# Kernel tuning notes

Measured on AMD Instinct MI355X. Metric: run time of the kernel, lower is better.

## Reference

```python
import jax, jax.numpy as jnp
import numpy as np

HEAD_DIM = 4  # hard-coded by rosa_4bit_layer's reshape(B, T, -1, 4)


def setup_inputs() -> dict:
    key = jax.random.key(0)
    B, T, C = 4, 4096, 512
    kq, kk, kv = jax.random.split(key, 3)
    xq = jax.random.normal(kq, (B, T, C), dtype=jnp.float32)
    xk = jax.random.normal(kk, (B, T, C), dtype=jnp.float32)
    xv = jax.random.normal(kv, (B, T, C), dtype=jnp.float32)
    emb = jnp.ones((1, 1, C), dtype=jnp.float32)  # nn.Parameter(torch.ones((1,1,C)))
    return {"xq": xq, "xk": xk, "xv": xv, "emb": emb}


def _rosa_sufa(q, k, v):
    # q,k,v: (B, H, T, d) with d = 4.
    # Causal linear-attention recurrence with per-head d x d state:
    #   S_t = S_{t-1} + k_t v_t^T ;  o_t = q_t^T S_t
    # expressed as a cumulative sum over outer products (vectorized over T).
    kv = jnp.cumsum(k[..., :, None] * v[..., None, :], axis=2)  # (B,H,T,d,d)
    return jnp.einsum('bhtd,bhtde->bhte', q, kv)                # (B,H,T,d)


def reference(xq, xk, xv, emb):
    B, T, C = xq.shape
    H = C // HEAD_DIM
    # (B,T,C) -> (B,T,H,4) -> (B,H,T,4)
    q = xq.reshape(B, T, H, HEAD_DIM).transpose(0, 2, 1, 3)
    k = xk.reshape(B, T, H, HEAD_DIM).transpose(0, 2, 1, 3)
    v = xv.reshape(B, T, H, HEAD_DIM).transpose(0, 2, 1, 3)
    o = _rosa_sufa(q, k, v)
    # (B,H,T,4) -> (B,T,C)
    o = o.transpose(0, 2, 1, 3).reshape(B, T, C)
    return o * emb
```

## Files before the change

kernel.cpp:

```cpp
#include <hip/hip_runtime.h>


constexpr int B  = 4;
constexpr int T  = 4096;
constexpr int C  = 512;
constexpr int CT = 32;
constexpr int NC = T / CT;

__global__ __launch_bounds__(512) void k_partial(const float* __restrict__ k,
                                                 const float* __restrict__ v,
                                                 float* __restrict__ part) {
  const int bc  = blockIdx.x;
  const int b   = bc / NC;
  const int c   = bc % NC;
  const int tid = threadIdx.x;
  const int h   = tid >> 2;
  const int e   = tid & 3;
  const int t0  = c * CT;

  const size_t base = ((size_t)b * T + t0) * (size_t)C + (h << 2);
  const float* kb = k + base;
  const float* vb = v + base + e;

  float4 acc = {0.f, 0.f, 0.f, 0.f};
#pragma unroll 8
  for (int t = 0; t < CT; ++t) {
    const float4 k4 = *reinterpret_cast<const float4*>(kb + (size_t)t * C);
    const float  ve = vb[(size_t)t * C];
    acc.x += k4.x * ve;
    acc.y += k4.y * ve;
    acc.z += k4.z * ve;
    acc.w += k4.w * ve;
  }
  reinterpret_cast<float4*>(part)[(size_t)bc * 512 + tid] = acc;
}

__global__ __launch_bounds__(256) void k_scan(float* __restrict__ part) {
  const int b = blockIdx.x >> 3;
  const int j = ((blockIdx.x & 7) << 8) + threadIdx.x;
  float run = 0.f;
  for (int c = 0; c < NC; ++c) {
    float* p = part + (size_t)(b * NC + c) * 2048 + j;
    const float val = *p;
    *p = run;
    run += val;
  }
}

__global__ __launch_bounds__(512) void k_out(const float* __restrict__ q,
                                             const float* __restrict__ k,
                                             const float* __restrict__ v,
                                             const float* __restrict__ emb,
                                             const float* __restrict__ part,
                                             float* __restrict__ out) {
  const int bc  = blockIdx.x;
  const int b   = bc / NC;
  const int c   = bc % NC;
  const int tid = threadIdx.x;
  const int h   = tid >> 2;
  const int e   = tid & 3;
  const int t0  = c * CT;

  const size_t base = ((size_t)b * T + t0) * (size_t)C + (h << 2);
  const float* qb = q + base;
  const float* kb = k + base;
  const float* vb = v + base + e;
  float*       ob = out + base + e;

  float4 S = reinterpret_cast<const float4*>(part)[(size_t)bc * 512 + tid];
  const float embv = emb[(h << 2) + e];

#pragma unroll 8
  for (int t = 0; t < CT; ++t) {
    const float4 k4 = *reinterpret_cast<const float4*>(kb + (size_t)t * C);
    const float4 q4 = *reinterpret_cast<const float4*>(qb + (size_t)t * C);
    const float  ve = vb[(size_t)t * C];
    S.x += k4.x * ve;
    S.y += k4.y * ve;
    S.z += k4.z * ve;
    S.w += k4.w * ve;
    const float o = q4.x * S.x + q4.y * S.y + q4.z * S.z + q4.w * S.w;
    ob[(size_t)t * C] = o * embv;
  }
}

extern "C" void kernel_launch(void* const* d_in, const int* in_sizes, int n_in,
                              void* d_out, int out_size, void* d_ws, size_t ws_size,
                              hipStream_t stream) {
  const float* xq  = (const float*)d_in[0];
  const float* xk  = (const float*)d_in[1];
  const float* xv  = (const float*)d_in[2];
  const float* emb = (const float*)d_in[3];
  float* out  = (float*)d_out;
  float* part = (float*)d_ws;

  k_partial<<<B * NC, 512, 0, stream>>>(xk, xv, part);
  k_scan<<<B * 8, 256, 0, stream>>>(part);
  k_out<<<B * NC, 512, 0, stream>>>(xq, xk, xv, emb, part, out);
}
```

Before: 151.2 us.

## Fuse chunk-state scan into output kernel via per-block prefix summation

Removes the separate serial scan kernel and instead has each output block sum all preceding chunk partial states itself before running its local recurrence. This eliminates one launch and the latency-bound serial scan pass. In exchange it performs quadratic redundant reads of the partial buffer, which are expected to hit in cache, and it creates load imbalance toward later chunks.

```diff
diff --git a/kernel.cpp b/kernel.cpp
--- a/kernel.cpp
+++ b/kernel.cpp
@@ -7,18 +7,17 @@
 constexpr int CT = 32;
 constexpr int NC = T / CT;
 
-__global__ __launch_bounds__(512) void k_partial(const float* __restrict__ k,
-                                                 const float* __restrict__ v,
-                                                 float* __restrict__ part) {
+__global__ __launch_bounds__(512) void rosa_partial(const float* __restrict__ k,
+                                                    const float* __restrict__ v,
+                                                    float* __restrict__ part) {
   const int bc  = blockIdx.x;
   const int b   = bc / NC;
   const int c   = bc % NC;
   const int tid = threadIdx.x;
   const int h   = tid >> 2;
   const int e   = tid & 3;
-  const int t0  = c * CT;
 
-  const size_t base = ((size_t)b * T + t0) * (size_t)C + (h << 2);
+  const size_t base = ((size_t)b * T + (size_t)c * CT) * (size_t)C + (h << 2);
   const float* kb = k + base;
   const float* vb = v + base + e;
 
@@ -35,39 +34,35 @@
   reinterpret_cast<float4*>(part)[(size_t)bc * 512 + tid] = acc;
 }
 
-__global__ __launch_bounds__(256) void k_scan(float* __restrict__ part) {
-  const int b = blockIdx.x >> 3;
-  const int j = ((blockIdx.x & 7) << 8) + threadIdx.x;
-  float run = 0.f;
-  for (int c = 0; c < NC; ++c) {
-    float* p = part + (size_t)(b * NC + c) * 2048 + j;
-    const float val = *p;
-    *p = run;
-    run += val;
-  }
-}
-
-__global__ __launch_bounds__(512) void k_out(const float* __restrict__ q,
-                                             const float* __restrict__ k,
-                                             const float* __restrict__ v,
-                                             const float* __restrict__ emb,
-                                             const float* __restrict__ part,
-                                             float* __restrict__ out) {
+__global__ __launch_bounds__(512) void rosa_scan_out(const float* __restrict__ q,
+                                                     const float* __restrict__ k,
+                                                     const float* __restrict__ v,
+                                                     const float* __restrict__ emb,
+                                                     const float* __restrict__ part,
+                                                     float* __restrict__ out) {
   const int bc  = blockIdx.x;
   const int b   = bc / NC;
   const int c   = bc % NC;
   const int tid = threadIdx.x;
   const int h   = tid >> 2;
   const int e   = tid & 3;
-  const int t0  = c * CT;
 
-  const size_t base = ((size_t)b * T + t0) * (size_t)C + (h << 2);
+  float4 S = {0.f, 0.f, 0.f, 0.f};
+  const float4* pb = reinterpret_cast<const float4*>(part) + (size_t)b * NC * 512 + tid;
+#pragma unroll 4
+  for (int cp = 0; cp < c; ++cp) {
+    const float4 p4 = pb[(size_t)cp * 512];
+    S.x += p4.x;
+    S.y += p4.y;
+    S.z += p4.z;
+    S.w += p4.w;
+  }
+
+  const size_t base = ((size_t)b * T + (size_t)c * CT) * (size_t)C + (h << 2);
   const float* qb = q + base;
   const float* kb = k + base;
   const float* vb = v + base + e;
   float*       ob = out + base + e;
-
-  float4 S = reinterpret_cast<const float4*>(part)[(size_t)bc * 512 + tid];
   const float embv = emb[(h << 2) + e];
 
 #pragma unroll 8
@@ -94,7 +89,6 @@
   float* out  = (float*)d_out;
   float* part = (float*)d_ws;
 
-  k_partial<<<B * NC, 512, 0, stream>>>(xk, xv, part);
-  k_scan<<<B * 8, 256, 0, stream>>>(part);
-  k_out<<<B * NC, 512, 0, stream>>>(xq, xk, xv, emb, part, out);
+  rosa_partial<<<B * NC, 512, 0, stream>>>(xk, xv, part);
+  rosa_scan_out<<<B * NC, 512, 0, stream>>>(xq, xk, xv, emb, part, out);
 }
```

Measured after the change: 164.1 us. +8.6%, slower.
